# Kernel tuning notes

Hardware: AMD Instinct MI355X
Metric: run time of the kernel (lower is better)

Reference implementation:

```python
import jax, jax.numpy as jnp
import numpy as np

N = 50000   # nodes
E = 200000  # triplets
IN = 128    # num_in_features
H = 4       # heads
F = 64      # num_out_features
HID = 64    # attention_mlp_hidden


def setup_inputs() -> dict:
    key = jax.random.key(0)
    ks = jax.random.split(key, 12)
    rn = lambda k, shape, s=0.05: (jax.random.normal(k, shape, jnp.float32) * s)
    return {
        "in_nodes_features": jax.random.normal(ks[0], (N, IN), jnp.float32),
        "edge_index": jax.random.randint(ks[1], (3, E), 0, N, jnp.int32),
        "W_proj": rn(ks[2], (H * F, IN)),          # linear_proj (no bias)
        "att_W1": rn(ks[3], (HID, 3 * F)),
        "att_b1": jnp.zeros((HID,), jnp.float32),
        "att_W2": rn(ks[4], (1, HID)),
        "att_b2": jnp.zeros((1,), jnp.float32),
        "e_W1": rn(ks[5], (F, 2 * F)),
        "e_b1": jnp.zeros((F,), jnp.float32),
        "e_W2": rn(ks[6], (F, F)),
        "e_b2": jnp.zeros((F,), jnp.float32),
        "theta": rn(ks[7], (1, H, F), 0.1),
        "bias": jnp.zeros((H * F,), jnp.float32),
    }


def _edge_nn(pair, e_W1, e_b1, e_W2, e_b2):
    # pair: [E, H, 2F] -> [E, H, F]
    h = jax.nn.leaky_relu(jnp.einsum('ehc,fc->ehf', pair, e_W1) + e_b1, 0.2)
    return jnp.einsum('ehf,gf->ehg', h, e_W2) + e_b2


def reference(in_nodes_features, edge_index, W_proj, att_W1, att_b1, att_W2,
              att_b2, e_W1, e_b1, e_W2, e_b2, theta, bias):
    proj = (in_nodes_features @ W_proj.T).reshape(-1, H, F)  # [N, H, F]
    pi = proj[edge_index[0]]  # [E, H, F]
    pj = proj[edge_index[1]]
    pk = proj[edge_index[2]]

    # attention MLP on concatenated triplet features
    comb = jnp.concatenate([pi, pj, pk], axis=-1)            # [E, H, 3F]
    h = jax.nn.relu(jnp.einsum('ehc,dc->ehd', comb, att_W1) + att_b1)
    scores = (jnp.einsum('ehd,od->eho', h, att_W2) + att_b2)[..., 0]  # [E, H]
    scores = jax.nn.leaky_relu(scores, 0.2)
    att = jax.nn.softmax(scores, axis=-1)[..., None]         # softmax over heads, [E, H, 1]

    pairs = [(pj, pk), (pi, pk), (pi, pj)]
    outs = []
    for i in range(3):
        prod = _edge_nn(jnp.concatenate(pairs[i], axis=-1), e_W1, e_b1, e_W2, e_b2)
        ws = jax.ops.segment_sum(att * prod, edge_index[i], num_segments=proj.shape[0])
        outs.append(theta * proj + ws)                       # [N, H, F]

    out = jnp.concatenate(outs, axis=0).reshape(-1, H * F)   # [3N, H*F]
    out = out + bias
    return jax.nn.elu(out)
```

## Files before the change

kernel.cpp:

```cpp
#include <hip/hip_runtime.h>
#include <hip/hip_bf16.h>

#define N_NODES 50000
#define N_EDGES 200000
#define IN_F 128
#define HEADS 4
#define FD 64
#define HF 256
#define NCOLS 1536
#define NT3 (3 * N_NODES)
#define E3  (3 * N_EDGES)
#define TROW 320

#define OFF_PROJ   0UL
#define OFF_TABS   51200000UL
#define OFF_ATT    179200000UL
#define OFF_RANK   182400000UL
#define OFF_ELIST2 184800000UL
#define OFF_CNT    194400000UL
#define OFF_OFFS   195000000UL
#define OFF_BSUM   195600008UL
#define OFF_BSW    195601040UL
#define OFF_CB     195994256UL

typedef __attribute__((ext_vector_type(8))) short short8;
typedef __attribute__((ext_vector_type(4))) float f32x4;

__device__ inline short bf16_of(float x) {
    __hip_bfloat16 h = __float2bfloat16(x);
    return *reinterpret_cast<short*>(&h);
}
__device__ inline unsigned pack2(float lo, float hi) {
    return ((unsigned)(unsigned short)bf16_of(hi) << 16) |
           (unsigned)(unsigned short)bf16_of(lo);
}
__device__ inline short8 pack8(float4 a, float4 b) {
    short8 o;
    o[0] = bf16_of(a.x); o[1] = bf16_of(a.y); o[2] = bf16_of(a.z); o[3] = bf16_of(a.w);
    o[4] = bf16_of(b.x); o[5] = bf16_of(b.y); o[6] = bf16_of(b.z); o[7] = bf16_of(b.w);
    return o;
}
__device__ inline void unpk(uint4 v, float* f) {
    f[0] = __uint_as_float(v.x << 16); f[1] = __uint_as_float(v.x & 0xffff0000u);
    f[2] = __uint_as_float(v.y << 16); f[3] = __uint_as_float(v.y & 0xffff0000u);
    f[4] = __uint_as_float(v.z << 16); f[5] = __uint_as_float(v.z & 0xffff0000u);
    f[6] = __uint_as_float(v.w << 16); f[7] = __uint_as_float(v.w & 0xffff0000u);
}
__device__ inline float score8(uint4 ua, uint4 ub, uint4 uc, const float* w) {
    float fa[8], fb[8], fc[8]; unpk(ua, fa); unpk(ub, fb); unpk(uc, fc);
    float p = 0.f;
#pragma unroll
    for (int j = 0; j < 8; ++j) {
        float x = fa[j] + fb[j] + fc[j];
        x = fmaxf(x, 0.f);
        p = fmaf(x, w[j], p);
    }
    return p;
}

__global__ __launch_bounds__(128) void k_comp(const float* __restrict__ Wp,
                                              const float* __restrict__ attW1,
                                              const float* __restrict__ eW1,
                                              const float* __restrict__ attb1,
                                              const float* __restrict__ eb1,
                                              __hip_bfloat16* __restrict__ Bsw,
                                              float* __restrict__ colbias) {
    const int c = blockIdx.x;
    const int k = threadIdx.x;
    float acc;
    float cb = 0.f;
    if (c < HF) {
        acc = Wp[c * IN_F + k];
    } else {
        const int t = (c - HF) >> 8;
        const int rem = (c - HF) & 255;
        const int h = rem >> 6, g = rem & 63;
        const float* T;
        if (t == 0)      T = attW1 + g * 192;
        else if (t == 1) T = attW1 + g * 192 + 64;
        else if (t == 2) T = attW1 + g * 192 + 128;
        else if (t == 3) T = eW1 + g * 128;
        else             T = eW1 + g * 128 + 64;
        acc = 0.f;
        for (int f = 0; f < 64; ++f)
            acc += T[f] * Wp[(h * 64 + f) * IN_F + k];
        if (t == 0) cb = attb1[g];
        else if (t == 3) cb = eb1[g];
    }
    const int ct = c >> 4, cin = c & 15, kin = k & 31, j = k & 7;
    const int ks = k >> 5;
    const int l = cin + ((kin >> 3) << 4);
    Bsw[((ct * 4 + ks) * 64 + l) * 8 + j] = __float2bfloat16(acc);
    if (k == 0) colbias[c] = cb;
}

__global__ __launch_bounds__(256) void k_tab(const float* __restrict__ in,
                                             const __hip_bfloat16* __restrict__ BswH,
                                             const float* __restrict__ colbias,
                                             float* __restrict__ proj,
                                             __hip_bfloat16* __restrict__ tabs) {
    __shared__ __hip_bfloat16 st_lds[4][16][20];
    const short8* Bsw = reinterpret_cast<const short8*>(BswH);
    const int lane = threadIdx.x & 63;
    const int wv = threadIdx.x >> 6;
    const int r = lane & 15, q = lane >> 4;
    const int row0 = blockIdx.x * 16;

    short8 a[4];
    const float* ip = in + (size_t)(row0 + r) * IN_F + q * 8;
#pragma unroll
    for (int ks = 0; ks < 4; ++ks)
        a[ks] = pack8(*(const float4*)(ip + ks * 32), *(const float4*)(ip + ks * 32 + 4));

    for (int ctl = 0; ctl < 24; ++ctl) {
        const int ct = wv * 24 + ctl;
        const int c = ct * 16 + r;
        const float cb = colbias[c];
        f32x4 acc = {cb, cb, cb, cb};
#pragma unroll
        for (int ks = 0; ks < 4; ++ks)
            acc = __builtin_amdgcn_mfma_f32_16x16x32_bf16(a[ks], Bsw[(ct * 4 + ks) * 64 + lane], acc, 0, 0, 0);
        if (c < HF) {
#pragma unroll
            for (int i = 0; i < 4; ++i)
                proj[(size_t)(row0 + q * 4 + i) * HF + c] = acc[i];
        } else {
#pragma unroll
            for (int i = 0; i < 4; ++i)
                st_lds[wv][q * 4 + i][r] = __float2bfloat16(acc[i]);
            const int rem0 = ct * 16 - HF;
            const int t = rem0 >> 8;
            const int h = (rem0 >> 6) & 3;
            const int g0 = rem0 & 63;
            const int rowl = lane >> 2, ch = lane & 3;
            uint2 val = *(const uint2*)&st_lds[wv][rowl][ch * 4];
            *(uint2*)(tabs + ((size_t)(row0 + rowl) * 4 + h) * TROW +
                      t * 64 + g0 + ch * 4) = val;
        }
    }
}

__global__ __launch_bounds__(256) void k_hist(const int* __restrict__ eidx,
                                              int* __restrict__ cnt,
                                              int* __restrict__ rank) {
    const int g = blockIdx.x * 256 + threadIdx.x;
    if (g < E3) {
        const int node = eidx[g];
        const int t = g / N_EDGES;
        rank[g] = atomicAdd(&cnt[t * N_NODES + node], 1);
    }
}

__global__ __launch_bounds__(256) void k_scan1(const int* __restrict__ cnt,
                                               int* __restrict__ offs,
                                               int* __restrict__ bsums) {
    __shared__ int lds[256];
    const int b = blockIdx.x, t = threadIdx.x;
    const int base = b * 1024 + t * 4;
    int v[4];
#pragma unroll
    for (int c = 0; c < 4; ++c) v[c] = (base + c < NT3) ? cnt[base + c] : 0;
    const int s = v[0] + v[1] + v[2] + v[3];
    lds[t] = s;
    __syncthreads();
    for (int off = 1; off < 256; off <<= 1) {
        int x = (t >= off) ? lds[t - off] : 0;
        __syncthreads();
        lds[t] += x;
        __syncthreads();
    }
    if (t == 255) bsums[b] = lds[255];
    int run = lds[t] - s;
#pragma unroll
    for (int c = 0; c < 4; ++c) {
        if (base + c < NT3) offs[base + c] = run;
        run += v[c];
    }
}

__global__ __launch_bounds__(256) void k_scan2(int* __restrict__ bsums, int nb) {
    __shared__ int lds[256];
    const int t = threadIdx.x;
    const int v = (t < nb) ? bsums[t] : 0;
    lds[t] = v;
    __syncthreads();
    for (int off = 1; off < 256; off <<= 1) {
        int x = (t >= off) ? lds[t - off] : 0;
        __syncthreads();
        lds[t] += x;
        __syncthreads();
    }
    if (t < nb) bsums[t] = lds[t] - v;
}

__global__ __launch_bounds__(256) void k_scan3(int* __restrict__ offs,
                                               const int* __restrict__ bsums) {
    const int i = blockIdx.x * 256 + threadIdx.x;
    if (i < NT3) offs[i] += bsums[i >> 10];
    if (i == NT3) offs[NT3] = E3;
}

__global__ __launch_bounds__(256) void k_scat(const int* __restrict__ eidx,
                                              const int* __restrict__ offs,
                                              const int* __restrict__ rank,
                                              int4* __restrict__ elist2) {
    const int g = blockIdx.x * 256 + threadIdx.x;
    if (g < E3) {
        const int node = eidx[g];
        const int t = g / N_EDGES;
        const int e = g - t * N_EDGES;
        const int s0 = (t == 0) ? 1 : 0;
        const int s1 = (t == 2) ? 1 : 2;
        const int x = eidx[s0 * N_EDGES + e];
        const int y = eidx[s1 * N_EDGES + e];
        elist2[offs[t * N_NODES + node] + rank[g]] = make_int4(x, y, e, 0);
    }
}

__global__ __launch_bounds__(256) void k_att(
        const int* __restrict__ eidx,
        const __hip_bfloat16* __restrict__ tabs,
        const float* __restrict__ attW2, const float* __restrict__ attb2,
        float* __restrict__ attbuf) {
    __shared__ float s_lds[HEADS][16];
    const int lane = threadIdx.x & 63;
    const int h = threadIdx.x >> 6;
    const int r = lane & 15, q = lane >> 4;
    const int e0 = blockIdx.x * 16;

    float awlo[8], awhi[8];
    {
        float4 w0 = *(const float4*)(attW2 + q * 8);
        float4 w1 = *(const float4*)(attW2 + q * 8 + 4);
        awlo[0] = w0.x; awlo[1] = w0.y; awlo[2] = w0.z; awlo[3] = w0.w;
        awlo[4] = w1.x; awlo[5] = w1.y; awlo[6] = w1.z; awlo[7] = w1.w;
        float4 w2 = *(const float4*)(attW2 + 32 + q * 8);
        float4 w3 = *(const float4*)(attW2 + 32 + q * 8 + 4);
        awhi[0] = w2.x; awhi[1] = w2.y; awhi[2] = w2.z; awhi[3] = w2.w;
        awhi[4] = w3.x; awhi[5] = w3.y; awhi[6] = w3.z; awhi[7] = w3.w;
    }
    const float ab2s = attb2[0];

    const int ni = eidx[e0 + r];
    const int nj = eidx[N_EDGES + e0 + r];
    const int nk = eidx[2 * N_EDGES + e0 + r];

    const size_t bi = ((size_t)ni * HEADS + h) * TROW + q * 8;
    const size_t bj = ((size_t)nj * HEADS + h) * TROW + q * 8;
    const size_t bk = ((size_t)nk * HEADS + h) * TROW + q * 8;

    uint4 a0 = *(const uint4*)(tabs + bi);
    uint4 a1 = *(const uint4*)(tabs + bi + 32);
    uint4 b0 = *(const uint4*)(tabs + bj + 64);
    uint4 b1 = *(const uint4*)(tabs + bj + 96);
    uint4 c0 = *(const uint4*)(tabs + bk + 128);
    uint4 c1 = *(const uint4*)(tabs + bk + 160);

    float p = score8(a0, b0, c0, awlo) + score8(a1, b1, c1, awhi);
    p += __shfl_xor(p, 16);
    p += __shfl_xor(p, 32);
    float sc = p + ab2s;
    sc = fmaxf(sc, 0.2f * sc);
    if (lane < 16) s_lds[h][lane] = sc;
    __syncthreads();
    if (lane < 16) {
        const float s0 = s_lds[0][lane], s1 = s_lds[1][lane];
        const float s2 = s_lds[2][lane], s3 = s_lds[3][lane];
        const float mx = fmaxf(fmaxf(s0, s1), fmaxf(s2, s3));
        const float x0 = __expf(s0 - mx), x1 = __expf(s1 - mx);
        const float x2 = __expf(s2 - mx), x3 = __expf(s3 - mx);
        const float rs = 1.f / (x0 + x1 + x2 + x3);
        const float xh = (h == 0) ? x0 : (h == 1) ? x1 : (h == 2) ? x2 : x3;
        attbuf[(size_t)(e0 + lane) * 4 + h] = xh * rs;
    }
}

__global__ __launch_bounds__(256) void k_seg(const int* __restrict__ offs,
                                             const int4* __restrict__ elist2,
                                             const float* __restrict__ attbuf,
                                             const __hip_bfloat16* __restrict__ tabs,
                                             const float* __restrict__ proj,
                                             const float* __restrict__ eW2,
                                             const float* __restrict__ eb2,
                                             const float* __restrict__ theta,
                                             const float* __restrict__ bias,
                                             float* __restrict__ out) {
    __shared__ __hip_bfloat16 S_lds[2][16][72];
    __shared__ float a_lds[2][16];
    __shared__ float D_lds[2][16][68];

    const int lane = threadIdx.x & 63;
    const int w = threadIdx.x >> 6;
    const int h = lane >> 4, r = lane & 15;
    const int q = lane >> 4;
    const int t = blockIdx.y;
    const int n0 = blockIdx.x * 8;
    const int idxA = t * N_NODES + n0 + w;
    const int idxB = idxA + 4;
    const int pA0 = offs[idxA], pA1 = offs[idxA + 1];
    const int pB0 = offs[idxB], pB1 = offs[idxB + 1];

    const int c1 = h * TROW + 192 + r * 4;
    const int c2 = h * TROW + 256 + r * 4;
    const int c_at = h;

    float aA0 = 0.f, aA1 = 0.f, aA2 = 0.f, aA3 = 0.f, alA = 0.f;
    float aB0 = 0.f, aB1 = 0.f, aB2 = 0.f, aB3 = 0.f, alB = 0.f;
    int baseA = pA0, baseB = pB0;
    while (baseA < pA1 || baseB < pB1) {
        int4 evA[4], evB[4];
#pragma unroll
        for (int c = 0; c < 4; ++c) {
            int pa = baseA + c;
            int ia = pa < pA1 ? pa : pA1 - 1; ia = ia < 0 ? 0 : ia;
            evA[c] = elist2[ia];
            int pb = baseB + c;
            int ib = pb < pB1 ? pb : pB1 - 1; ib = ib < 0 ? 0 : ib;
            evB[c] = elist2[ib];
        }
        int xA[4], yA[4], zA[4], xB[4], yB[4], zB[4];
#pragma unroll
        for (int c = 0; c < 4; ++c) {
            xA[c] = __builtin_amdgcn_readfirstlane(evA[c].x);
            yA[c] = __builtin_amdgcn_readfirstlane(evA[c].y);
            zA[c] = __builtin_amdgcn_readfirstlane(evA[c].z);
            xB[c] = __builtin_amdgcn_readfirstlane(evB[c].x);
            yB[c] = __builtin_amdgcn_readfirstlane(evB[c].y);
            zB[c] = __builtin_amdgcn_readfirstlane(evB[c].z);
        }
        float atA[4], atB[4];
#pragma unroll
        for (int c = 0; c < 4; ++c) {
            atA[c] = (baseA + c < pA1) ? attbuf[(size_t)zA[c] * 4 + c_at] : 0.f;
            atB[c] = (baseB + c < pB1) ? attbuf[(size_t)zB[c] * 4 + c_at] : 0.f;
        }
        uint2 uaA[4], ubA[4], uaB[4], ubB[4];
#pragma unroll
        for (int c = 0; c < 4; ++c) {
            uaA[c] = *(const uint2*)(tabs + (size_t)xA[c] * 1280 + c1);
            ubA[c] = *(const uint2*)(tabs + (size_t)yA[c] * 1280 + c2);
            uaB[c] = *(const uint2*)(tabs + (size_t)xB[c] * 1280 + c1);
            ubB[c] = *(const uint2*)(tabs + (size_t)yB[c] * 1280 + c2);
        }
#pragma unroll
        for (int c = 0; c < 4; ++c) {
            float g0 = __uint_as_float(uaA[c].x << 16) + __uint_as_float(ubA[c].x << 16);
            float g1 = __uint_as_float(uaA[c].x & 0xffff0000u) + __uint_as_float(ubA[c].x & 0xffff0000u);
            float g2 = __uint_as_float(uaA[c].y << 16) + __uint_as_float(ubA[c].y << 16);
            float g3 = __uint_as_float(uaA[c].y & 0xffff0000u) + __uint_as_float(ubA[c].y & 0xffff0000u);
            g0 = fmaxf(g0, 0.2f * g0); g1 = fmaxf(g1, 0.2f * g1);
            g2 = fmaxf(g2, 0.2f * g2); g3 = fmaxf(g3, 0.2f * g3);
            aA0 = fmaf(atA[c], g0, aA0); aA1 = fmaf(atA[c], g1, aA1);
            aA2 = fmaf(atA[c], g2, aA2); aA3 = fmaf(atA[c], g3, aA3);
            alA += atA[c];
        }
#pragma unroll
        for (int c = 0; c < 4; ++c) {
            float g0 = __uint_as_float(uaB[c].x << 16) + __uint_as_float(ubB[c].x << 16);
            float g1 = __uint_as_float(uaB[c].x & 0xffff0000u) + __uint_as_float(ubB[c].x & 0xffff0000u);
            float g2 = __uint_as_float(uaB[c].y << 16) + __uint_as_float(ubB[c].y << 16);
            float g3 = __uint_as_float(uaB[c].y & 0xffff0000u) + __uint_as_float(ubB[c].y & 0xffff0000u);
            g0 = fmaxf(g0, 0.2f * g0); g1 = fmaxf(g1, 0.2f * g1);
            g2 = fmaxf(g2, 0.2f * g2); g3 = fmaxf(g3, 0.2f * g3);
            aB0 = fmaf(atB[c], g0, aB0); aB1 = fmaf(atB[c], g1, aB1);
            aB2 = fmaf(atB[c], g2, aB2); aB3 = fmaf(atB[c], g3, aB3);
            alB += atB[c];
        }
        baseA += 4; baseB += 4;
    }
    const int tr = w * 4 + h;
    {
        uint2 st;
        st.x = pack2(aA0, aA1); st.y = pack2(aA2, aA3);
        *(uint2*)&S_lds[0][tr][r * 4] = st;
        st.x = pack2(aB0, aB1); st.y = pack2(aB2, aB3);
        *(uint2*)&S_lds[1][tr][r * 4] = st;
        if (r == 0) { a_lds[0][tr] = alA; a_lds[1][tr] = alB; }
    }
    __syncthreads();

    {
        const float* wp0 = eW2 + (w * 16 + r) * FD + q * 8;
        const float* wp1 = eW2 + (w * 16 + r) * FD + 32 + q * 8;
        short8 bfr0 = pack8(*(const float4*)wp0, *(const float4*)(wp0 + 4));
        short8 bfr1 = pack8(*(const float4*)wp1, *(const float4*)(wp1 + 4));
#pragma unroll
        for (int k = 0; k < 2; ++k) {
            short8 A0 = *(short8*)&S_lds[k][r][q * 8];
            short8 A1 = *(short8*)&S_lds[k][r][32 + q * 8];
            f32x4 acc = {0.f, 0.f, 0.f, 0.f};
            acc = __builtin_amdgcn_mfma_f32_16x16x32_bf16(A0, bfr0, acc, 0, 0, 0);
            acc = __builtin_amdgcn_mfma_f32_16x16x32_bf16(A1, bfr1, acc, 0, 0, 0);
#pragma unroll
            for (int i = 0; i < 4; ++i)
                D_lds[k][q * 4 + i][w * 16 + r] = acc[i];
        }
    }
    __syncthreads();

    const int row = threadIdx.x >> 4;
    const int c4 = threadIdx.x & 15;
    const int f = c4 * 4;
    const int hh = row & 3;
    float4 th = *(const float4*)(theta + hh * 64 + f);
    float4 bi = *(const float4*)(bias + hh * 64 + f);
    float4 b2 = *(const float4*)(eb2 + f);
#pragma unroll
    for (int k = 0; k < 2; ++k) {
        const int nn = n0 + k * 4 + (row >> 2);
        const size_t rho = ((size_t)t * N_NODES + nn) * 4 + hh;
        float4 Dv = *(float4*)&D_lds[k][row][f];
        float4 pj = *(const float4*)(proj + (size_t)nn * HF + hh * 64 + f);
        const float al = a_lds[k][row];
        float4 o;
        float v;
        v = th.x * pj.x + Dv.x + al * b2.x + bi.x; o.x = v > 0.f ? v : expm1f(v);
        v = th.y * pj.y + Dv.y + al * b2.y + bi.y; o.y = v > 0.f ? v : expm1f(v);
        v = th.z * pj.z + Dv.z + al * b2.z + bi.z; o.z = v > 0.f ? v : expm1f(v);
        v = th.w * pj.w + Dv.w + al * b2.w + bi.w; o.w = v > 0.f ? v : expm1f(v);
        *(float4*)(out + rho * 64 + f) = o;
    }
}

extern "C" void kernel_launch(void* const* d_in, const int* in_sizes, int n_in,
                              void* d_out, int out_size, void* d_ws, size_t ws_size,
                              hipStream_t stream) {
    const float* in_nodes = (const float*)d_in[0];
    const int*   eidx     = (const int*)d_in[1];
    const float* Wp       = (const float*)d_in[2];
    const float* attW1    = (const float*)d_in[3];
    const float* attb1    = (const float*)d_in[4];
    const float* attW2    = (const float*)d_in[5];
    const float* attb2    = (const float*)d_in[6];
    const float* eW1      = (const float*)d_in[7];
    const float* eb1      = (const float*)d_in[8];
    const float* eW2      = (const float*)d_in[9];
    const float* eb2      = (const float*)d_in[10];
    const float* theta    = (const float*)d_in[11];
    const float* bias     = (const float*)d_in[12];

    char* ws = (char*)d_ws;
    float*          proj     = (float*)(ws + OFF_PROJ);
    __hip_bfloat16* tabs     = (__hip_bfloat16*)(ws + OFF_TABS);
    float*          attbuf   = (float*)(ws + OFF_ATT);
    int*            rank     = (int*)(ws + OFF_RANK);
    int4*           elist2   = (int4*)(ws + OFF_ELIST2);
    int*            cnt      = (int*)(ws + OFF_CNT);
    int*            offs     = (int*)(ws + OFF_OFFS);
    int*            bsums    = (int*)(ws + OFF_BSUM);
    __hip_bfloat16* Bsw      = (__hip_bfloat16*)(ws + OFF_BSW);
    float*          colbias  = (float*)(ws + OFF_CB);

    float* out = (float*)d_out;

    (void)hipMemsetAsync(cnt, 0, NT3 * sizeof(int), stream);

    k_comp<<<NCOLS, 128, 0, stream>>>(Wp, attW1, eW1, attb1, eb1, Bsw, colbias);
    k_tab<<<N_NODES / 16, 256, 0, stream>>>(in_nodes, Bsw, colbias, proj, tabs);

    k_hist<<<(E3 + 255) / 256, 256, 0, stream>>>(eidx, cnt, rank);
    k_scan1<<<(NT3 + 1023) / 1024, 256, 0, stream>>>(cnt, offs, bsums);
    k_scan2<<<1, 256, 0, stream>>>(bsums, (NT3 + 1023) / 1024);
    k_scan3<<<(NT3 + 256) / 256, 256, 0, stream>>>(offs, bsums);
    k_scat<<<(E3 + 255) / 256, 256, 0, stream>>>(eidx, offs, rank, elist2);

    k_att<<<N_EDGES / 16, 256, 0, stream>>>(eidx, tabs, attW2, attb2, attbuf);
    k_seg<<<dim3(N_NODES / 8, 3), 256, 0, stream>>>(offs, elist2, attbuf,
                                                    tabs, proj, eW2, eb2,
                                                    theta, bias, out);
}
```

Baseline: 348.9 us.

## Pre-scatter attention weights into CSR order and split edge list into xy pairs

Moves the attention kernel ahead of the scatter step so the scatter can copy each edge's four head weights into a segment-sorted array next to a compact (x,y) int2 list. The segment-sum kernel then reads attention weights contiguously by list position instead of doing a dependent gather through the edge id, and loads 8-byte entries instead of 16-byte ones. The attention kernel also handles two 16-edge groups per block, halving its block count. The cost is an extra 16-byte write and read per triplet slot in the scatter kernel, plus more workspace.

```diff
diff --git a/kernel.cpp b/kernel.cpp
--- a/kernel.cpp
+++ b/kernel.cpp
@@ -16,12 +16,13 @@
 #define OFF_TABS   51200000UL
 #define OFF_ATT    179200000UL
 #define OFF_RANK   182400000UL
-#define OFF_ELIST2 184800000UL
-#define OFF_CNT    194400000UL
-#define OFF_OFFS   195000000UL
-#define OFF_BSUM   195600008UL
-#define OFF_BSW    195601040UL
-#define OFF_CB     195994256UL
+#define OFF_XY     184800000UL
+#define OFF_ATTS   189600000UL
+#define OFF_CNT    199200000UL
+#define OFF_OFFS   199800000UL
+#define OFF_BSUM   200400008UL
+#define OFF_BSW    200401040UL
+#define OFF_CB     200794256UL
 
 typedef __attribute__((ext_vector_type(8))) short short8;
 typedef __attribute__((ext_vector_type(4))) float f32x4;
@@ -203,7 +204,9 @@
 __global__ __launch_bounds__(256) void k_scat(const int* __restrict__ eidx,
                                               const int* __restrict__ offs,
                                               const int* __restrict__ rank,
-                                              int4* __restrict__ elist2) {
+                                              const float* __restrict__ attbuf,
+                                              int2* __restrict__ xy,
+                                              float* __restrict__ atts) {
     const int g = blockIdx.x * 256 + threadIdx.x;
     if (g < E3) {
         const int node = eidx[g];
@@ -213,7 +216,10 @@
         const int s1 = (t == 2) ? 1 : 2;
         const int x = eidx[s0 * N_EDGES + e];
         const int y = eidx[s1 * N_EDGES + e];
-        elist2[offs[t * N_NODES + node] + rank[g]] = make_int4(x, y, e, 0);
+        const int dest = offs[t * N_NODES + node] + rank[g];
+        xy[dest] = make_int2(x, y);
+        const float4 a4 = *(const float4*)(attbuf + (size_t)e * 4);
+        *(float4*)(atts + (size_t)dest * 4) = a4;
     }
 }
 
@@ -226,7 +232,6 @@
     const int lane = threadIdx.x & 63;
     const int h = threadIdx.x >> 6;
     const int r = lane & 15, q = lane >> 4;
-    const int e0 = blockIdx.x * 16;
 
     float awlo[8], awhi[8];
     {
@@ -241,43 +246,49 @@
     }
     const float ab2s = attb2[0];
 
-    const int ni = eidx[e0 + r];
-    const int nj = eidx[N_EDGES + e0 + r];
-    const int nk = eidx[2 * N_EDGES + e0 + r];
-
-    const size_t bi = ((size_t)ni * HEADS + h) * TROW + q * 8;
-    const size_t bj = ((size_t)nj * HEADS + h) * TROW + q * 8;
-    const size_t bk = ((size_t)nk * HEADS + h) * TROW + q * 8;
-
-    uint4 a0 = *(const uint4*)(tabs + bi);
-    uint4 a1 = *(const uint4*)(tabs + bi + 32);
-    uint4 b0 = *(const uint4*)(tabs + bj + 64);
-    uint4 b1 = *(const uint4*)(tabs + bj + 96);
-    uint4 c0 = *(const uint4*)(tabs + bk + 128);
-    uint4 c1 = *(const uint4*)(tabs + bk + 160);
-
-    float p = score8(a0, b0, c0, awlo) + score8(a1, b1, c1, awhi);
-    p += __shfl_xor(p, 16);
-    p += __shfl_xor(p, 32);
-    float sc = p + ab2s;
-    sc = fmaxf(sc, 0.2f * sc);
-    if (lane < 16) s_lds[h][lane] = sc;
-    __syncthreads();
-    if (lane < 16) {
-        const float s0 = s_lds[0][lane], s1 = s_lds[1][lane];
-        const float s2 = s_lds[2][lane], s3 = s_lds[3][lane];
-        const float mx = fmaxf(fmaxf(s0, s1), fmaxf(s2, s3));
-        const float x0 = __expf(s0 - mx), x1 = __expf(s1 - mx);
-        const float x2 = __expf(s2 - mx), x3 = __expf(s3 - mx);
-        const float rs = 1.f / (x0 + x1 + x2 + x3);
-        const float xh = (h == 0) ? x0 : (h == 1) ? x1 : (h == 2) ? x2 : x3;
-        attbuf[(size_t)(e0 + lane) * 4 + h] = xh * rs;
+#pragma unroll
+    for (int s = 0; s < 2; ++s) {
+        const int e0 = blockIdx.x * 32 + s * 16;
+        if (s) __syncthreads();
+
+        const int ni = eidx[e0 + r];
+        const int nj = eidx[N_EDGES + e0 + r];
+        const int nk = eidx[2 * N_EDGES + e0 + r];
+
+        const size_t bi = ((size_t)ni * HEADS + h) * TROW + q * 8;
+        const size_t bj = ((size_t)nj * HEADS + h) * TROW + q * 8;
+        const size_t bk = ((size_t)nk * HEADS + h) * TROW + q * 8;
+
+        uint4 a0 = *(const uint4*)(tabs + bi);
+        uint4 a1 = *(const uint4*)(tabs + bi + 32);
+        uint4 b0 = *(const uint4*)(tabs + bj + 64);
+        uint4 b1 = *(const uint4*)(tabs + bj + 96);
+        uint4 c0 = *(const uint4*)(tabs + bk + 128);
+        uint4 c1 = *(const uint4*)(tabs + bk + 160);
+
+        float p = score8(a0, b0, c0, awlo) + score8(a1, b1, c1, awhi);
+        p += __shfl_xor(p, 16);
+        p += __shfl_xor(p, 32);
+        float sc = p + ab2s;
+        sc = fmaxf(sc, 0.2f * sc);
+        if (lane < 16) s_lds[h][lane] = sc;
+        __syncthreads();
+        if (lane < 16) {
+            const float s0 = s_lds[0][lane], s1 = s_lds[1][lane];
+            const float s2 = s_lds[2][lane], s3 = s_lds[3][lane];
+            const float mx = fmaxf(fmaxf(s0, s1), fmaxf(s2, s3));
+            const float x0 = __expf(s0 - mx), x1 = __expf(s1 - mx);
+            const float x2 = __expf(s2 - mx), x3 = __expf(s3 - mx);
+            const float rs = 1.f / (x0 + x1 + x2 + x3);
+            const float xh = (h == 0) ? x0 : (h == 1) ? x1 : (h == 2) ? x2 : x3;
+            attbuf[(size_t)(e0 + lane) * 4 + h] = xh * rs;
+        }
     }
 }
 
 __global__ __launch_bounds__(256) void k_seg(const int* __restrict__ offs,
-                                             const int4* __restrict__ elist2,
-                                             const float* __restrict__ attbuf,
+                                             const int2* __restrict__ xy,
+                                             const float* __restrict__ atts,
                                              const __hip_bfloat16* __restrict__ tabs,
                                              const float* __restrict__ proj,
                                              const float* __restrict__ eW2,
@@ -302,37 +313,35 @@
 
     const int c1 = h * TROW + 192 + r * 4;
     const int c2 = h * TROW + 256 + r * 4;
-    const int c_at = h;
 
     float aA0 = 0.f, aA1 = 0.f, aA2 = 0.f, aA3 = 0.f, alA = 0.f;
     float aB0 = 0.f, aB1 = 0.f, aB2 = 0.f, aB3 = 0.f, alB = 0.f;
     int baseA = pA0, baseB = pB0;
     while (baseA < pA1 || baseB < pB1) {
-        int4 evA[4], evB[4];
+        int2 xyA[4], xyB[4];
+        int iaA[4], iaB[4];
 #pragma unroll
         for (int c = 0; c < 4; ++c) {
             int pa = baseA + c;
             int ia = pa < pA1 ? pa : pA1 - 1; ia = ia < 0 ? 0 : ia;
-            evA[c] = elist2[ia];
+            iaA[c] = ia; xyA[c] = xy[ia];
             int pb = baseB + c;
             int ib = pb < pB1 ? pb : pB1 - 1; ib = ib < 0 ? 0 : ib;
-            evB[c] = elist2[ib];
-        }
-        int xA[4], yA[4], zA[4], xB[4], yB[4], zB[4];
-#pragma unroll
-        for (int c = 0; c < 4; ++c) {
-            xA[c] = __builtin_amdgcn_readfirstlane(evA[c].x);
-            yA[c] = __builtin_amdgcn_readfirstlane(evA[c].y);
-            zA[c] = __builtin_amdgcn_readfirstlane(evA[c].z);
-            xB[c] = __builtin_amdgcn_readfirstlane(evB[c].x);
-            yB[c] = __builtin_amdgcn_readfirstlane(evB[c].y);
-            zB[c] = __builtin_amdgcn_readfirstlane(evB[c].z);
+            iaB[c] = ib; xyB[c] = xy[ib];
         }
         float atA[4], atB[4];
 #pragma unroll
         for (int c = 0; c < 4; ++c) {
-            atA[c] = (baseA + c < pA1) ? attbuf[(size_t)zA[c] * 4 + c_at] : 0.f;
-            atB[c] = (baseB + c < pB1) ? attbuf[(size_t)zB[c] * 4 + c_at] : 0.f;
+            atA[c] = (baseA + c < pA1) ? atts[(size_t)iaA[c] * 4 + h] : 0.f;
+            atB[c] = (baseB + c < pB1) ? atts[(size_t)iaB[c] * 4 + h] : 0.f;
+        }
+        int xA[4], yA[4], xB[4], yB[4];
+#pragma unroll
+        for (int c = 0; c < 4; ++c) {
+            xA[c] = __builtin_amdgcn_readfirstlane(xyA[c].x);
+            yA[c] = __builtin_amdgcn_readfirstlane(xyA[c].y);
+            xB[c] = __builtin_amdgcn_readfirstlane(xyB[c].x);
+            yB[c] = __builtin_amdgcn_readfirstlane(xyB[c].y);
         }
         uint2 uaA[4], ubA[4], uaB[4], ubB[4];
 #pragma unroll
@@ -444,7 +453,8 @@
     __hip_bfloat16* tabs     = (__hip_bfloat16*)(ws + OFF_TABS);
     float*          attbuf   = (float*)(ws + OFF_ATT);
     int*            rank     = (int*)(ws + OFF_RANK);
-    int4*           elist2   = (int4*)(ws + OFF_ELIST2);
+    int2*           xy       = (int2*)(ws + OFF_XY);
+    float*          atts     = (float*)(ws + OFF_ATTS);
     int*            cnt      = (int*)(ws + OFF_CNT);
     int*            offs     = (int*)(ws + OFF_OFFS);
     int*            bsums    = (int*)(ws + OFF_BSUM);
@@ -462,10 +472,11 @@
     k_scan1<<<(NT3 + 1023) / 1024, 256, 0, stream>>>(cnt, offs, bsums);
     k_scan2<<<1, 256, 0, stream>>>(bsums, (NT3 + 1023) / 1024);
     k_scan3<<<(NT3 + 256) / 256, 256, 0, stream>>>(offs, bsums);
-    k_scat<<<(E3 + 255) / 256, 256, 0, stream>>>(eidx, offs, rank, elist2);
-
-    k_att<<<N_EDGES / 16, 256, 0, stream>>>(eidx, tabs, attW2, attb2, attbuf);
-    k_seg<<<dim3(N_NODES / 8, 3), 256, 0, stream>>>(offs, elist2, attbuf,
+
+    k_att<<<N_EDGES / 32, 256, 0, stream>>>(eidx, tabs, attW2, attb2, attbuf);
+    k_scat<<<(E3 + 255) / 256, 256, 0, stream>>>(eidx, offs, rank, attbuf, xy, atts);
+
+    k_seg<<<dim3(N_NODES / 8, 3), 256, 0, stream>>>(offs, xy, atts,
                                                     tabs, proj, eW2, eb2,
                                                     theta, bias, out);
 }
```

Result: no change. 353.8 us (+1.4%).
